# Kernel tuning notes

Measured on AMD Instinct MI355X. Metric: run time of the kernel, lower is better.

The kernel has to match this reference:

```python
import jax, jax.numpy as jnp
import numpy as np

N_NODES = 100000


def gcn_conv(x, edge_index, W, b, num_nodes):
    """PyG GCNConv: add self-loops, symmetric deg^{-1/2} normalization,
    aggregate (x @ W) over edges, then add bias."""
    loop = jnp.arange(num_nodes, dtype=edge_index.dtype)
    src = jnp.concatenate([edge_index[0], loop])  # [E+N]
    dst = jnp.concatenate([edge_index[1], loop])
    deg = jax.ops.segment_sum(jnp.ones_like(dst, dtype=x.dtype), dst,
                              num_segments=num_nodes)  # in-degree incl. self-loop
    dinv = jnp.where(deg > 0, jax.lax.rsqrt(deg), 0.0)
    norm = dinv[src] * dinv[dst]  # [E+N]
    h = x @ W  # [N, F_out] -- transform BEFORE gather (small F_out)
    msg = h[src] * norm[:, None]  # [E+N, F_out]
    out = jax.ops.segment_sum(msg, dst, num_segments=num_nodes)
    return out + b


def setup_inputs() -> dict:
    key = jax.random.key(0)
    k1, k2, k3, k4 = jax.random.split(key, 4)
    N, E, F_in, F_hid, F_out = N_NODES, 3200000, 128, 16, 64
    x = jax.random.normal(k1, (N, F_in), dtype=jnp.float32)
    edge_index = jax.random.randint(k2, (2, E), 0, N, dtype=jnp.int64)
    # glorot-ish init for weights, zeros bias (PyG default: glorot W, zeros b)
    W1 = jax.random.normal(k3, (F_in, F_hid), dtype=jnp.float32) * (1.0 / np.sqrt(F_in))
    b1 = jnp.zeros((F_hid,), dtype=jnp.float32)
    W2 = jax.random.normal(k4, (F_hid, F_out), dtype=jnp.float32) * (1.0 / np.sqrt(F_hid))
    b2 = jnp.zeros((F_out,), dtype=jnp.float32)
    return {"x": x, "edge_index": edge_index, "W1": W1, "b1": b1, "W2": W2, "b2": b2}


def reference(x, edge_index, W1, b1, W2, b2):
    N = x.shape[0]
    h = gcn_conv(x, edge_index, W1, b1, N)
    h = jax.nn.relu(h)
    # F.dropout with training=False (inference) is identity
    h = gcn_conv(h, edge_index, W2, b2, N)
    return jax.nn.log_softmax(h, axis=1)
```

## Files before the change

### kernel.cpp

```cpp
#include <hip/hip_runtime.h>

#define FIN 128
#define FH  16
#define FO  64
#define GB  128
#define MAXNB 1024
#define CHUNK 16384

__device__ __forceinline__ unsigned pack_bf16x2(float a, float b) {
    unsigned ua = __float_as_uint(a), ub = __float_as_uint(b);
    ua = (ua + 0x7fffu + ((ua >> 16) & 1u)) >> 16;
    ub = (ub + 0x7fffu + ((ub >> 16) & 1u)) >> 16;
    return ua | (ub << 16);
}

__device__ __forceinline__ float2 unpack_bf16x2(unsigned u) {
    float2 r;
    r.x = __uint_as_float(u << 16);
    r.y = __uint_as_float(u & 0xffff0000u);
    return r;
}

__global__ __launch_bounds__(1024) void k_bscatter(const int* __restrict__ src,
                                                   const int* __restrict__ dst,
                                                   int* __restrict__ bfill,
                                                   int* __restrict__ bedge,
                                                   int E, int slab) {
    __shared__ int h[MAXNB];
    __shared__ int scanp[1024];
    __shared__ int stage[CHUNK];
    int t = threadIdx.x;
    int c0 = blockIdx.x * CHUNK;
    int c1 = min(c0 + CHUNK, E);

    h[t] = 0;
    __syncthreads();
    const int4* dst4 = (const int4*)dst;
    const int4* src4 = (const int4*)src;
    int i4b = c0 >> 2;
    int i4e = (c0 + ((c1 - c0) & ~3)) >> 2;
    for (int i = i4b + t; i < i4e; i += 1024) {
        int4 d = dst4[i];
        atomicAdd(&h[d.x >> 7], 1);
        atomicAdd(&h[d.y >> 7], 1);
        atomicAdd(&h[d.z >> 7], 1);
        atomicAdd(&h[d.w >> 7], 1);
    }
    for (int e = (i4e << 2) + t; e < c1; e += 1024)
        atomicAdd(&h[dst[e] >> 7], 1);
    __syncthreads();

    int a = h[t];
    scanp[t] = a;
    __syncthreads();
    for (int off = 1; off < 1024; off <<= 1) {
        int u = (t >= off) ? scanp[t - off] : 0;
        __syncthreads();
        scanp[t] += u;
        __syncthreads();
    }
    int lo = scanp[t] - a;

    int r = 0;
    if (a) r = atomicAdd(&bfill[t], a);
    int navail = slab - r; if (navail < 0) navail = 0;
    int hi = lo + min(a, navail);
    h[t] = lo;
    __syncthreads();

    for (int i = i4b + t; i < i4e; i += 1024) {
        int4 d = dst4[i];
        int4 s = src4[i];
        int p;
        p = atomicAdd(&h[d.x >> 7], 1); stage[p] = ((d.x & 127) << 17) | s.x;
        p = atomicAdd(&h[d.y >> 7], 1); stage[p] = ((d.y & 127) << 17) | s.y;
        p = atomicAdd(&h[d.z >> 7], 1); stage[p] = ((d.z & 127) << 17) | s.z;
        p = atomicAdd(&h[d.w >> 7], 1); stage[p] = ((d.w & 127) << 17) | s.w;
    }
    for (int e = (i4e << 2) + t; e < c1; e += 1024) {
        int d = dst[e];
        int p = atomicAdd(&h[d >> 7], 1);
        stage[p] = ((d & 127) << 17) | src[e];
    }
    __syncthreads();

    int db = t * slab + r - lo;
    int p = lo;
    for (; p < hi && ((db + p) & 3); ++p) bedge[db + p] = stage[p];
    for (; p + 3 < hi; p += 4) {
        int4 v;
        v.x = stage[p]; v.y = stage[p + 1]; v.z = stage[p + 2]; v.w = stage[p + 3];
        *(int4*)(bedge + db + p) = v;
    }
    for (; p < hi; ++p) bedge[db + p] = stage[p];
}

__global__ __launch_bounds__(256) void k_nsg(const int* __restrict__ bfill,
                                             const int* __restrict__ bedge,
                                             const float* __restrict__ x,
                                             const float* __restrict__ W1,
                                             int* __restrict__ sorted_src,
                                             int* __restrict__ counts,
                                             int* __restrict__ row_start,
                                             float* __restrict__ dinv,
                                             uint2* __restrict__ hs1u2,
                                             int N, int slab) {
    __shared__ int hist[GB];
    __shared__ int fill[GB];
    __shared__ float dinvL[GB];
    __shared__ float4 w4[FIN * FH / 4];
    int t = threadIdx.x, b = blockIdx.x;
    int base = b << 7;
    int nn = min(GB, N - base);
    if (nn <= 0) return;

    int ebeg = b * slab;
    int eend = ebeg + min(bfill[b], slab);
    if (t < GB) hist[t] = 0;
    __syncthreads();
    for (int e = ebeg + t; e < eend; e += 256)
        atomicAdd(&hist[bedge[e] >> 17], 1);
    __syncthreads();
    int c = (t < GB) ? hist[t] : 0;
    for (int off = 1; off < GB; off <<= 1) {
        int u = (t < GB && t >= off) ? hist[t - off] : 0;
        __syncthreads();
        if (t < GB) hist[t] += u;
        __syncthreads();
    }
    int excl = (t < GB) ? hist[t] - c : 0;
    if (t < nn) {
        counts[base + t] = c;
        row_start[base + t] = ebeg + excl;
        float dv = rsqrtf((float)(c + 1));
        dinv[base + t] = dv;
        dinvL[t] = dv;
        fill[t] = ebeg + excl;
    }
    __syncthreads();
    for (int e = ebeg + t; e < eend; e += 256) {
        int v = bedge[e];
        int p = atomicAdd(&fill[v >> 17], 1);
        sorted_src[p] = v & 0x1FFFF;
    }
    for (int i = t; i < FIN * FH / 4; i += 256) w4[i] = ((const float4*)W1)[i];
    __syncthreads();

    int fg = t & 3, rg = t >> 2;
    int r0l = rg * 2;
    if (r0l >= nn) return;
    int r1l = min(r0l + 1, nn - 1);
    int r0 = base + r0l, r1 = base + r1l;
    const float4* xa4 = (const float4*)(x + (long long)r0 * FIN);
    const float4* xb4 = (const float4*)(x + (long long)r1 * FIN);
    float4 a0 = make_float4(0.f, 0.f, 0.f, 0.f);
    float4 a1 = make_float4(0.f, 0.f, 0.f, 0.f);
#pragma unroll 2
    for (int k4 = 0; k4 < FIN / 4; ++k4) {
        float4 xa = xa4[k4];
        float4 xb = xb4[k4];
        const float4* wp = &w4[k4 * 16 + fg];
        float4 w0 = wp[0], w1 = wp[4], w2 = wp[8], w3 = wp[12];
        a0.x = fmaf(xa.x, w0.x, a0.x); a0.y = fmaf(xa.x, w0.y, a0.y);
        a0.z = fmaf(xa.x, w0.z, a0.z); a0.w = fmaf(xa.x, w0.w, a0.w);
        a0.x = fmaf(xa.y, w1.x, a0.x); a0.y = fmaf(xa.y, w1.y, a0.y);
        a0.z = fmaf(xa.y, w1.z, a0.z); a0.w = fmaf(xa.y, w1.w, a0.w);
        a0.x = fmaf(xa.z, w2.x, a0.x); a0.y = fmaf(xa.z, w2.y, a0.y);
        a0.z = fmaf(xa.z, w2.z, a0.z); a0.w = fmaf(xa.z, w2.w, a0.w);
        a0.x = fmaf(xa.w, w3.x, a0.x); a0.y = fmaf(xa.w, w3.y, a0.y);
        a0.z = fmaf(xa.w, w3.z, a0.z); a0.w = fmaf(xa.w, w3.w, a0.w);
        a1.x = fmaf(xb.x, w0.x, a1.x); a1.y = fmaf(xb.x, w0.y, a1.y);
        a1.z = fmaf(xb.x, w0.z, a1.z); a1.w = fmaf(xb.x, w0.w, a1.w);
        a1.x = fmaf(xb.y, w1.x, a1.x); a1.y = fmaf(xb.y, w1.y, a1.y);
        a1.z = fmaf(xb.y, w1.z, a1.z); a1.w = fmaf(xb.y, w1.w, a1.w);
        a1.x = fmaf(xb.z, w2.x, a1.x); a1.y = fmaf(xb.z, w2.y, a1.y);
        a1.z = fmaf(xb.z, w2.z, a1.z); a1.w = fmaf(xb.z, w2.w, a1.w);
        a1.x = fmaf(xb.w, w3.x, a1.x); a1.y = fmaf(xb.w, w3.y, a1.y);
        a1.z = fmaf(xb.w, w3.z, a1.z); a1.w = fmaf(xb.w, w3.w, a1.w);
    }
    float d0 = dinvL[r0l];
    uint2 o0;
    o0.x = pack_bf16x2(a0.x * d0, a0.y * d0);
    o0.y = pack_bf16x2(a0.z * d0, a0.w * d0);
    hs1u2[r0 * 4 + fg] = o0;
    if (r1l != r0l) {
        float d1 = dinvL[r1l];
        uint2 o1;
        o1.x = pack_bf16x2(a1.x * d1, a1.y * d1);
        o1.y = pack_bf16x2(a1.z * d1, a1.w * d1);
        hs1u2[r1 * 4 + fg] = o1;
    }
}

__global__ __launch_bounds__(256) void k_gather1(const int* __restrict__ rs,
                                                 const int* __restrict__ cnt,
                                                 const int* __restrict__ ss,
                                                 const unsigned* __restrict__ hs1u,
                                                 const float* __restrict__ dinv,
                                                 const float* __restrict__ b1,
                                                 unsigned* __restrict__ h1su, int n) {
    int t = threadIdx.x;
    int lane = t & 63;
    int l32 = lane & 31, g4 = l32 >> 3, f2 = l32 & 7;
    int node = blockIdx.x * 8 + ((t >> 6) << 1) + (lane >> 5);
    bool act = (node < n);
    int beg = 0, end = 0;
    unsigned uself = 0;
    float di = 0.0f;
    if (act) {
        beg = rs[node]; end = beg + cnt[node];
        uself = hs1u[node * 8 + f2];
        di = dinv[node];
    }
    float ax = 0.0f, ay = 0.0f;
    int e = beg + g4;
    for (; e + 28 < end; e += 32) {
        int s0 = ss[e],      s1 = ss[e + 4],  s2 = ss[e + 8],  s3 = ss[e + 12];
        int s4 = ss[e + 16], s5 = ss[e + 20], s6 = ss[e + 24], s7 = ss[e + 28];
        unsigned u0 = hs1u[s0 * 8 + f2], u1 = hs1u[s1 * 8 + f2];
        unsigned u2 = hs1u[s2 * 8 + f2], u3 = hs1u[s3 * 8 + f2];
        unsigned u4 = hs1u[s4 * 8 + f2], u5 = hs1u[s5 * 8 + f2];
        unsigned u6 = hs1u[s6 * 8 + f2], u7 = hs1u[s7 * 8 + f2];
        float2 p0 = unpack_bf16x2(u0), p1 = unpack_bf16x2(u1);
        float2 p2 = unpack_bf16x2(u2), p3 = unpack_bf16x2(u3);
        float2 p4 = unpack_bf16x2(u4), p5 = unpack_bf16x2(u5);
        float2 p6 = unpack_bf16x2(u6), p7 = unpack_bf16x2(u7);
        ax += ((p0.x + p1.x) + (p2.x + p3.x)) + ((p4.x + p5.x) + (p6.x + p7.x));
        ay += ((p0.y + p1.y) + (p2.y + p3.y)) + ((p4.y + p5.y) + (p6.y + p7.y));
    }
    for (; e + 4 < end; e += 8) {
        int s0 = ss[e], s1 = ss[e + 4];
        unsigned u0 = hs1u[s0 * 8 + f2], u1 = hs1u[s1 * 8 + f2];
        float2 p0 = unpack_bf16x2(u0), p1 = unpack_bf16x2(u1);
        ax += p0.x + p1.x; ay += p0.y + p1.y;
    }
    if (e < end) {
        float2 p = unpack_bf16x2(hs1u[ss[e] * 8 + f2]);
        ax += p.x; ay += p.y;
    }
    ax += __shfl_xor(ax, 8, 64);  ay += __shfl_xor(ay, 8, 64);
    ax += __shfl_xor(ax, 16, 64); ay += __shfl_xor(ay, 16, 64);
    if (act) {
        float2 s = unpack_bf16x2(uself);
        ax += s.x; ay += s.y;
        float2 bb = ((const float2*)b1)[f2];
        float v0 = fmaxf(fmaf(di, ax, bb.x), 0.0f) * di;
        float v1 = fmaxf(fmaf(di, ay, bb.y), 0.0f) * di;
        if (l32 < 8) h1su[node * 8 + f2] = pack_bf16x2(v0, v1);
    }
}

__global__ __launch_bounds__(256) void k_agg2f(const int* __restrict__ rs,
                                               const int* __restrict__ cnt,
                                               const int* __restrict__ ss,
                                               const unsigned* __restrict__ h1su,
                                               const float* __restrict__ dinv,
                                               const float* __restrict__ W2,
                                               const float* __restrict__ b2,
                                               float* __restrict__ out, int n) {
    int t = threadIdx.x;
    int lane = t & 63;
    int l32 = lane & 31, g4 = l32 >> 3, f2 = l32 & 7;
    int node = blockIdx.x * 8 + ((t >> 6) << 1) + (lane >> 5);
    bool act = (node < n);
    int beg = 0, end = 0;
    unsigned uself = 0;
    float di = 0.0f;
    if (act) {
        beg = rs[node]; end = beg + cnt[node];
        uself = h1su[node * 8 + f2];
        di = dinv[node];
    }
    float ax = 0.0f, ay = 0.0f;
    int e = beg + g4;
    for (; e + 28 < end; e += 32) {
        int s0 = ss[e],      s1 = ss[e + 4],  s2 = ss[e + 8],  s3 = ss[e + 12];
        int s4 = ss[e + 16], s5 = ss[e + 20], s6 = ss[e + 24], s7 = ss[e + 28];
        unsigned u0 = h1su[s0 * 8 + f2], u1 = h1su[s1 * 8 + f2];
        unsigned u2 = h1su[s2 * 8 + f2], u3 = h1su[s3 * 8 + f2];
        unsigned u4 = h1su[s4 * 8 + f2], u5 = h1su[s5 * 8 + f2];
        unsigned u6 = h1su[s6 * 8 + f2], u7 = h1su[s7 * 8 + f2];
        float2 p0 = unpack_bf16x2(u0), p1 = unpack_bf16x2(u1);
        float2 p2 = unpack_bf16x2(u2), p3 = unpack_bf16x2(u3);
        float2 p4 = unpack_bf16x2(u4), p5 = unpack_bf16x2(u5);
        float2 p6 = unpack_bf16x2(u6), p7 = unpack_bf16x2(u7);
        ax += ((p0.x + p1.x) + (p2.x + p3.x)) + ((p4.x + p5.x) + (p6.x + p7.x));
        ay += ((p0.y + p1.y) + (p2.y + p3.y)) + ((p4.y + p5.y) + (p6.y + p7.y));
    }
    for (; e + 4 < end; e += 8) {
        int s0 = ss[e], s1 = ss[e + 4];
        unsigned u0 = h1su[s0 * 8 + f2], u1 = h1su[s1 * 8 + f2];
        float2 p0 = unpack_bf16x2(u0), p1 = unpack_bf16x2(u1);
        ax += p0.x + p1.x; ay += p0.y + p1.y;
    }
    if (e < end) {
        float2 p = unpack_bf16x2(h1su[ss[e] * 8 + f2]);
        ax += p.x; ay += p.y;
    }
    ax += __shfl_xor(ax, 8, 64);  ay += __shfl_xor(ay, 8, 64);
    ax += __shfl_xor(ax, 16, 64); ay += __shfl_xor(ay, 16, 64);
    float2 s = unpack_bf16x2(uself);
    ax += s.x; ay += s.y;
    float w0[FH], w1[FH];
#pragma unroll
    for (int j = 0; j < FH; ++j) {
        w0[j] = W2[j * FO + l32];
        w1[j] = W2[j * FO + l32 + 32];
    }
    float o0 = 0.0f, o1 = 0.0f;
#pragma unroll
    for (int j = 0; j < 8; ++j) {
        float gx = __shfl(ax, j, 8), gy = __shfl(ay, j, 8);
        o0 = fmaf(gx, w0[2 * j], o0); o0 = fmaf(gy, w0[2 * j + 1], o0);
        o1 = fmaf(gx, w1[2 * j], o1); o1 = fmaf(gy, w1[2 * j + 1], o1);
    }
    float v0 = fmaf(di, o0, b2[l32]);
    float v1 = fmaf(di, o1, b2[l32 + 32]);
    float m = fmaxf(v0, v1);
#pragma unroll
    for (int off = 16; off >= 1; off >>= 1) m = fmaxf(m, __shfl_xor(m, off, 64));
    float ex = __expf(v0 - m) + __expf(v1 - m);
#pragma unroll
    for (int off = 16; off >= 1; off >>= 1) ex += __shfl_xor(ex, off, 64);
    float lse = m + __logf(ex);
    if (act) {
        float* orow = out + (long long)node * FO;
        orow[l32]      = v0 - lse;
        orow[l32 + 32] = v1 - lse;
    }
}

extern "C" void kernel_launch(void* const* d_in, const int* in_sizes, int n_in,
                              void* d_out, int out_size, void* d_ws, size_t ws_size,
                              hipStream_t stream) {
    const float* x  = (const float*)d_in[0];
    const int*   ei = (const int*)d_in[1];
    const float* W1 = (const float*)d_in[2];
    const float* b1 = (const float*)d_in[3];
    const float* W2 = (const float*)d_in[4];
    const float* b2 = (const float*)d_in[5];
    float* out = (float*)d_out;

    int N = in_sizes[0] / FIN;
    int E = in_sizes[1] / 2;
    const int* src = ei;
    const int* dst = ei + E;
    int nb = (N + GB - 1) / GB;

    int slab = (E + nb - 1) / nb;
    slab = slab + slab / 4 + 1024;
    slab = (slab + 15) & ~15;
    long long slabtot = (long long)nb * slab;

    unsigned* hs1u  = (unsigned*)d_ws;
    unsigned* h1su  = hs1u + 8LL * N;
    int* bfill      = (int*)(h1su + 8LL * N);
    int* counts     = bfill + MAXNB;
    int* row_start  = counts + N;
    int* sorted_src = row_start + N;
    int* bedge      = sorted_src + slabtot;
    float* dinv     = (float*)(bedge + slabtot);

    hipMemsetAsync(bfill, 0, MAXNB * sizeof(int), stream);
    k_bscatter<<<(E + CHUNK - 1) / CHUNK, 1024, 0, stream>>>(src, dst, bfill, bedge, E, slab);
    k_nsg<<<nb, 256, 0, stream>>>(bfill, bedge, x, W1, sorted_src, counts, row_start,
                                  dinv, (uint2*)hs1u, N, slab);
    k_gather1<<<(N + 7) / 8, 256, 0, stream>>>(row_start, counts, sorted_src, hs1u, dinv, b1, h1su, N);
    k_agg2f<<<(N + 7) / 8, 256, 0, stream>>>(row_start, counts, sorted_src, h1su, dinv, W2, b2, out, N);
}
```

Baseline: 236.2 us.

## Halve lanes per node in gathers and widen k_nsg to 512 threads

The two edge-gather kernels now use 16 lanes per node (2 edge groups × 8 feature pairs) instead of 32, so each wavefront handles 4 nodes and the launch covers 16 nodes per block. In the final kernel each lane now computes 4 output columns, and the log-softmax reductions shrink to a 16-lane span. k_nsg moves to 512 threads with one row per 4-thread group instead of two, which gives the sort phase more threads and less per-thread work in the x@W1 transform. The aim is less lane idling on short adjacency lists (average degree ~32) at the cost of fewer loads in flight per node and more per-lane compute in the W2 projection.

```diff
diff --git a/kernel.cpp b/kernel.cpp
--- a/kernel.cpp
+++ b/kernel.cpp
@@ -95,7 +95,7 @@
     for (; p < hi; ++p) bedge[db + p] = stage[p];
 }
 
-__global__ __launch_bounds__(256) void k_nsg(const int* __restrict__ bfill,
+__global__ __launch_bounds__(512) void k_nsg(const int* __restrict__ bfill,
                                              const int* __restrict__ bedge,
                                              const float* __restrict__ x,
                                              const float* __restrict__ W1,
@@ -118,7 +118,7 @@
     int eend = ebeg + min(bfill[b], slab);
     if (t < GB) hist[t] = 0;
     __syncthreads();
-    for (int e = ebeg + t; e < eend; e += 256)
+    for (int e = ebeg + t; e < eend; e += 512)
         atomicAdd(&hist[bedge[e] >> 17], 1);
     __syncthreads();
     int c = (t < GB) ? hist[t] : 0;
@@ -138,27 +138,22 @@
         fill[t] = ebeg + excl;
     }
     __syncthreads();
-    for (int e = ebeg + t; e < eend; e += 256) {
+    for (int e = ebeg + t; e < eend; e += 512) {
         int v = bedge[e];
         int p = atomicAdd(&fill[v >> 17], 1);
         sorted_src[p] = v & 0x1FFFF;
     }
-    for (int i = t; i < FIN * FH / 4; i += 256) w4[i] = ((const float4*)W1)[i];
+    for (int i = t; i < FIN * FH / 4; i += 512) w4[i] = ((const float4*)W1)[i];
     __syncthreads();
 
     int fg = t & 3, rg = t >> 2;
-    int r0l = rg * 2;
-    if (r0l >= nn) return;
-    int r1l = min(r0l + 1, nn - 1);
-    int r0 = base + r0l, r1 = base + r1l;
+    if (rg >= nn) return;
+    int r0 = base + rg;
     const float4* xa4 = (const float4*)(x + (long long)r0 * FIN);
-    const float4* xb4 = (const float4*)(x + (long long)r1 * FIN);
     float4 a0 = make_float4(0.f, 0.f, 0.f, 0.f);
-    float4 a1 = make_float4(0.f, 0.f, 0.f, 0.f);
-#pragma unroll 2
+#pragma unroll 4
     for (int k4 = 0; k4 < FIN / 4; ++k4) {
         float4 xa = xa4[k4];
-        float4 xb = xb4[k4];
         const float4* wp = &w4[k4 * 16 + fg];
         float4 w0 = wp[0], w1 = wp[4], w2 = wp[8], w3 = wp[12];
         a0.x = fmaf(xa.x, w0.x, a0.x); a0.y = fmaf(xa.x, w0.y, a0.y);
@@ -169,27 +164,12 @@
         a0.z = fmaf(xa.z, w2.z, a0.z); a0.w = fmaf(xa.z, w2.w, a0.w);
         a0.x = fmaf(xa.w, w3.x, a0.x); a0.y = fmaf(xa.w, w3.y, a0.y);
         a0.z = fmaf(xa.w, w3.z, a0.z); a0.w = fmaf(xa.w, w3.w, a0.w);
-        a1.x = fmaf(xb.x, w0.x, a1.x); a1.y = fmaf(xb.x, w0.y, a1.y);
-        a1.z = fmaf(xb.x, w0.z, a1.z); a1.w = fmaf(xb.x, w0.w, a1.w);
-        a1.x = fmaf(xb.y, w1.x, a1.x); a1.y = fmaf(xb.y, w1.y, a1.y);
-        a1.z = fmaf(xb.y, w1.z, a1.z); a1.w = fmaf(xb.y, w1.w, a1.w);
-        a1.x = fmaf(xb.z, w2.x, a1.x); a1.y = fmaf(xb.z, w2.y, a1.y);
-        a1.z = fmaf(xb.z, w2.z, a1.z); a1.w = fmaf(xb.z, w2.w, a1.w);
-        a1.x = fmaf(xb.w, w3.x, a1.x); a1.y = fmaf(xb.w, w3.y, a1.y);
-        a1.z = fmaf(xb.w, w3.z, a1.z); a1.w = fmaf(xb.w, w3.w, a1.w);
-    }
-    float d0 = dinvL[r0l];
+    }
+    float d0 = dinvL[rg];
     uint2 o0;
     o0.x = pack_bf16x2(a0.x * d0, a0.y * d0);
     o0.y = pack_bf16x2(a0.z * d0, a0.w * d0);
     hs1u2[r0 * 4 + fg] = o0;
-    if (r1l != r0l) {
-        float d1 = dinvL[r1l];
-        uint2 o1;
-        o1.x = pack_bf16x2(a1.x * d1, a1.y * d1);
-        o1.y = pack_bf16x2(a1.z * d1, a1.w * d1);
-        hs1u2[r1 * 4 + fg] = o1;
-    }
 }
 
 __global__ __launch_bounds__(256) void k_gather1(const int* __restrict__ rs,
@@ -201,8 +181,8 @@
                                                  unsigned* __restrict__ h1su, int n) {
     int t = threadIdx.x;
     int lane = t & 63;
-    int l32 = lane & 31, g4 = l32 >> 3, f2 = l32 & 7;
-    int node = blockIdx.x * 8 + ((t >> 6) << 1) + (lane >> 5);
+    int l16 = lane & 15, g2 = l16 >> 3, f2 = l16 & 7;
+    int node = blockIdx.x * 16 + ((t >> 6) << 2) + (lane >> 4);
     bool act = (node < n);
     int beg = 0, end = 0;
     unsigned uself = 0;
@@ -213,10 +193,10 @@
         di = dinv[node];
     }
     float ax = 0.0f, ay = 0.0f;
-    int e = beg + g4;
-    for (; e + 28 < end; e += 32) {
-        int s0 = ss[e],      s1 = ss[e + 4],  s2 = ss[e + 8],  s3 = ss[e + 12];
-        int s4 = ss[e + 16], s5 = ss[e + 20], s6 = ss[e + 24], s7 = ss[e + 28];
+    int e = beg + g2;
+    for (; e + 14 < end; e += 16) {
+        int s0 = ss[e],      s1 = ss[e + 2],  s2 = ss[e + 4],  s3 = ss[e + 6];
+        int s4 = ss[e + 8],  s5 = ss[e + 10], s6 = ss[e + 12], s7 = ss[e + 14];
         unsigned u0 = hs1u[s0 * 8 + f2], u1 = hs1u[s1 * 8 + f2];
         unsigned u2 = hs1u[s2 * 8 + f2], u3 = hs1u[s3 * 8 + f2];
         unsigned u4 = hs1u[s4 * 8 + f2], u5 = hs1u[s5 * 8 + f2];
@@ -228,8 +208,17 @@
         ax += ((p0.x + p1.x) + (p2.x + p3.x)) + ((p4.x + p5.x) + (p6.x + p7.x));
         ay += ((p0.y + p1.y) + (p2.y + p3.y)) + ((p4.y + p5.y) + (p6.y + p7.y));
     }
-    for (; e + 4 < end; e += 8) {
-        int s0 = ss[e], s1 = ss[e + 4];
+    for (; e + 6 < end; e += 8) {
+        int s0 = ss[e], s1 = ss[e + 2], s2 = ss[e + 4], s3 = ss[e + 6];
+        unsigned u0 = hs1u[s0 * 8 + f2], u1 = hs1u[s1 * 8 + f2];
+        unsigned u2 = hs1u[s2 * 8 + f2], u3 = hs1u[s3 * 8 + f2];
+        float2 p0 = unpack_bf16x2(u0), p1 = unpack_bf16x2(u1);
+        float2 p2 = unpack_bf16x2(u2), p3 = unpack_bf16x2(u3);
+        ax += (p0.x + p1.x) + (p2.x + p3.x);
+        ay += (p0.y + p1.y) + (p2.y + p3.y);
+    }
+    for (; e + 2 < end; e += 4) {
+        int s0 = ss[e], s1 = ss[e + 2];
         unsigned u0 = hs1u[s0 * 8 + f2], u1 = hs1u[s1 * 8 + f2];
         float2 p0 = unpack_bf16x2(u0), p1 = unpack_bf16x2(u1);
         ax += p0.x + p1.x; ay += p0.y + p1.y;
@@ -239,14 +228,13 @@
         ax += p.x; ay += p.y;
     }
     ax += __shfl_xor(ax, 8, 64);  ay += __shfl_xor(ay, 8, 64);
-    ax += __shfl_xor(ax, 16, 64); ay += __shfl_xor(ay, 16, 64);
     if (act) {
         float2 s = unpack_bf16x2(uself);
         ax += s.x; ay += s.y;
         float2 bb = ((const float2*)b1)[f2];
         float v0 = fmaxf(fmaf(di, ax, bb.x), 0.0f) * di;
         float v1 = fmaxf(fmaf(di, ay, bb.y), 0.0f) * di;
-        if (l32 < 8) h1su[node * 8 + f2] = pack_bf16x2(v0, v1);
+        if (l16 < 8) h1su[node * 8 + f2] = pack_bf16x2(v0, v1);
     }
 }
 
@@ -260,8 +248,8 @@
                                                float* __restrict__ out, int n) {
     int t = threadIdx.x;
     int lane = t & 63;
-    int l32 = lane & 31, g4 = l32 >> 3, f2 = l32 & 7;
-    int node = blockIdx.x * 8 + ((t >> 6) << 1) + (lane >> 5);
+    int l16 = lane & 15, g2 = l16 >> 3, f2 = l16 & 7;
+    int node = blockIdx.x * 16 + ((t >> 6) << 2) + (lane >> 4);
     bool act = (node < n);
     int beg = 0, end = 0;
     unsigned uself = 0;
@@ -272,10 +260,10 @@
         di = dinv[node];
     }
     float ax = 0.0f, ay = 0.0f;
-    int e = beg + g4;
-    for (; e + 28 < end; e += 32) {
-        int s0 = ss[e],      s1 = ss[e + 4],  s2 = ss[e + 8],  s3 = ss[e + 12];
-        int s4 = ss[e + 16], s5 = ss[e + 20], s6 = ss[e + 24], s7 = ss[e + 28];
+    int e = beg + g2;
+    for (; e + 14 < end; e += 16) {
+        int s0 = ss[e],      s1 = ss[e + 2],  s2 = ss[e + 4],  s3 = ss[e + 6];
+        int s4 = ss[e + 8],  s5 = ss[e + 10], s6 = ss[e + 12], s7 = ss[e + 14];
         unsigned u0 = h1su[s0 * 8 + f2], u1 = h1su[s1 * 8 + f2];
         unsigned u2 = h1su[s2 * 8 + f2], u3 = h1su[s3 * 8 + f2];
         unsigned u4 = h1su[s4 * 8 + f2], u5 = h1su[s5 * 8 + f2];
@@ -287,8 +275,17 @@
         ax += ((p0.x + p1.x) + (p2.x + p3.x)) + ((p4.x + p5.x) + (p6.x + p7.x));
         ay += ((p0.y + p1.y) + (p2.y + p3.y)) + ((p4.y + p5.y) + (p6.y + p7.y));
     }
-    for (; e + 4 < end; e += 8) {
-        int s0 = ss[e], s1 = ss[e + 4];
+    for (; e + 6 < end; e += 8) {
+        int s0 = ss[e], s1 = ss[e + 2], s2 = ss[e + 4], s3 = ss[e + 6];
+        unsigned u0 = h1su[s0 * 8 + f2], u1 = h1su[s1 * 8 + f2];
+        unsigned u2 = h1su[s2 * 8 + f2], u3 = h1su[s3 * 8 + f2];
+        float2 p0 = unpack_bf16x2(u0), p1 = unpack_bf16x2(u1);
+        float2 p2 = unpack_bf16x2(u2), p3 = unpack_bf16x2(u3);
+        ax += (p0.x + p1.x) + (p2.x + p3.x);
+        ay += (p0.y + p1.y) + (p2.y + p3.y);
+    }
+    for (; e + 2 < end; e += 4) {
+        int s0 = ss[e], s1 = ss[e + 2];
         unsigned u0 = h1su[s0 * 8 + f2], u1 = h1su[s1 * 8 + f2];
         float2 p0 = unpack_bf16x2(u0), p1 = unpack_bf16x2(u1);
         ax += p0.x + p1.x; ay += p0.y + p1.y;
@@ -298,35 +295,54 @@
         ax += p.x; ay += p.y;
     }
     ax += __shfl_xor(ax, 8, 64);  ay += __shfl_xor(ay, 8, 64);
-    ax += __shfl_xor(ax, 16, 64); ay += __shfl_xor(ay, 16, 64);
     float2 s = unpack_bf16x2(uself);
     ax += s.x; ay += s.y;
+    float gg[FH];
+#pragma unroll
+    for (int j = 0; j < 8; ++j) {
+        gg[2 * j]     = __shfl(ax, j, 8);
+        gg[2 * j + 1] = __shfl(ay, j, 8);
+    }
     float w0[FH], w1[FH];
 #pragma unroll
     for (int j = 0; j < FH; ++j) {
-        w0[j] = W2[j * FO + l32];
-        w1[j] = W2[j * FO + l32 + 32];
+        w0[j] = W2[j * FO + l16];
+        w1[j] = W2[j * FO + l16 + 16];
     }
     float o0 = 0.0f, o1 = 0.0f;
 #pragma unroll
-    for (int j = 0; j < 8; ++j) {
-        float gx = __shfl(ax, j, 8), gy = __shfl(ay, j, 8);
-        o0 = fmaf(gx, w0[2 * j], o0); o0 = fmaf(gy, w0[2 * j + 1], o0);
-        o1 = fmaf(gx, w1[2 * j], o1); o1 = fmaf(gy, w1[2 * j + 1], o1);
-    }
-    float v0 = fmaf(di, o0, b2[l32]);
-    float v1 = fmaf(di, o1, b2[l32 + 32]);
-    float m = fmaxf(v0, v1);
-#pragma unroll
-    for (int off = 16; off >= 1; off >>= 1) m = fmaxf(m, __shfl_xor(m, off, 64));
-    float ex = __expf(v0 - m) + __expf(v1 - m);
-#pragma unroll
-    for (int off = 16; off >= 1; off >>= 1) ex += __shfl_xor(ex, off, 64);
+    for (int j = 0; j < FH; ++j) {
+        o0 = fmaf(gg[j], w0[j], o0);
+        o1 = fmaf(gg[j], w1[j], o1);
+    }
+#pragma unroll
+    for (int j = 0; j < FH; ++j) {
+        w0[j] = W2[j * FO + l16 + 32];
+        w1[j] = W2[j * FO + l16 + 48];
+    }
+    float o2 = 0.0f, o3 = 0.0f;
+#pragma unroll
+    for (int j = 0; j < FH; ++j) {
+        o2 = fmaf(gg[j], w0[j], o2);
+        o3 = fmaf(gg[j], w1[j], o3);
+    }
+    float v0 = fmaf(di, o0, b2[l16]);
+    float v1 = fmaf(di, o1, b2[l16 + 16]);
+    float v2 = fmaf(di, o2, b2[l16 + 32]);
+    float v3 = fmaf(di, o3, b2[l16 + 48]);
+    float m = fmaxf(fmaxf(v0, v1), fmaxf(v2, v3));
+#pragma unroll
+    for (int off = 8; off >= 1; off >>= 1) m = fmaxf(m, __shfl_xor(m, off, 64));
+    float ex = __expf(v0 - m) + __expf(v1 - m) + __expf(v2 - m) + __expf(v3 - m);
+#pragma unroll
+    for (int off = 8; off >= 1; off >>= 1) ex += __shfl_xor(ex, off, 64);
     float lse = m + __logf(ex);
     if (act) {
         float* orow = out + (long long)node * FO;
-        orow[l32]      = v0 - lse;
-        orow[l32 + 32] = v1 - lse;
+        orow[l16]      = v0 - lse;
+        orow[l16 + 16] = v1 - lse;
+        orow[l16 + 32] = v2 - lse;
+        orow[l16 + 48] = v3 - lse;
     }
 }
 
@@ -363,8 +379,8 @@
 
     hipMemsetAsync(bfill, 0, MAXNB * sizeof(int), stream);
     k_bscatter<<<(E + CHUNK - 1) / CHUNK, 1024, 0, stream>>>(src, dst, bfill, bedge, E, slab);
-    k_nsg<<<nb, 256, 0, stream>>>(bfill, bedge, x, W1, sorted_src, counts, row_start,
+    k_nsg<<<nb, 512, 0, stream>>>(bfill, bedge, x, W1, sorted_src, counts, row_start,
                                   dinv, (uint2*)hs1u, N, slab);
-    k_gather1<<<(N + 7) / 8, 256, 0, stream>>>(row_start, counts, sorted_src, hs1u, dinv, b1, h1su, N);
-    k_agg2f<<<(N + 7) / 8, 256, 0, stream>>>(row_start, counts, sorted_src, h1su, dinv, W2, b2, out, N);
-}
+    k_gather1<<<(N + 15) / 16, 256, 0, stream>>>(row_start, counts, sorted_src, hs1u, dinv, b1, h1su, N);
+    k_agg2f<<<(N + 15) / 16, 256, 0, stream>>>(row_start, counts, sorted_src, h1su, dinv, W2, b2, out, N);
+}
```

New measurement: 228.7 us. -3.2%, faster.
